# Kernel optimization log

Hardware: AMD Instinct MI355X
Metric: run time of the kernel (lower is better)

The kernel has to match this reference:

```python
import math
import jax, jax.numpy as jnp
import numpy as np


def _unfold(x, kh, kw, dh, dw, ph, pw):
    """F.unfold equivalent: returns (n, c, kh*kw, h, w), channel-major like torch."""
    n, c, h, w = x.shape
    xp = jnp.pad(x, ((0, 0), (0, 0), (ph, ph), (pw, pw)))
    patches = jnp.stack(
        [xp[:, :, i * dh:i * dh + h, j * dw:j * dw + w]
         for i in range(kh) for j in range(kw)],
        axis=2,
    )
    return patches  # (n, c, kh*kw, h, w)


def setup_inputs() -> dict:
    key = jax.random.key(0)
    k1, k2, k3, k4 = jax.random.split(key, 4)
    n, c, h, w = 8, 128, 64, 64
    x = jax.random.normal(k1, (n, c, h, w), dtype=jnp.float32)
    p1_w = 0.1 * jax.random.normal(k2, (1, c, h, 1), dtype=jnp.float32)  # trunc_normal std=0.1
    p7_w = jax.random.normal(k3, (c, c), dtype=jnp.float32) / np.sqrt(c)  # 1x1 conv c->c
    # grouped 1x1 conv: groups=4, out=c*21, weight (c*21, c//4)
    p10_w = jax.random.normal(k4, (c * 21, c // 4), dtype=jnp.float32) / np.sqrt(c // 4)
    return {"x": x, "p1_w": p1_w, "p7_w": p7_w, "p10_w": p10_w}


def reference(x, p1_w, p7_w, p10_w):
    n, c, h, w = x.shape
    g = 4
    t1 = p1_w * x                        # (n,c,h,w)
    t2 = x + t1
    t4 = jax.nn.relu(x)
    t5 = _unfold(x, 3, 7, 1, 1, 1, 3)    # (n,c,21,h,w)
    t7 = jnp.einsum('oc,nchw->nohw', p7_w, t4)        # 1x1 conv
    t8 = _unfold(t7, 1, 5, 1, 3, 0, 6)   # (n,c,5,h,w)
    t9 = x[:, :, None] - t8              # (n,c,5,h,w)
    # grouped 1x1 conv c -> c*21, groups=4
    xg = t2.reshape(n, g, c // g, h, w)
    wg = p10_w.reshape(g, (c * 21) // g, c // g)
    t10 = jnp.einsum('ngihw,goi->ngohw', xg, wg).reshape(n, c * 21, h, w)
    # score: (n,c,hw) x (n,hw,c*21) -> (n,c,c*21)
    t1f = t1.reshape(n, c, h * w)
    t5f = t5.reshape(n, c * 21, h * w)
    t11 = jnp.einsum('nck,nmk->ncm', t1f, t5f) / math.sqrt(h * w)
    t12 = t9.mean(2)                     # (n,c,h,w)
    t13 = jnp.einsum('ncm,nmk->nck', t11, t10.reshape(n, c * 21, h * w))
    t13 = t13.reshape(n, c, h, w) / math.sqrt(c * 21)
    return jnp.maximum(t13, t12)
```

## Files before the change

kernel.cpp:

```cpp
#include <hip/hip_runtime.h>
#include <hip/hip_bf16.h>

typedef unsigned short ushort_t;
typedef unsigned int uint_t;
typedef __attribute__((ext_vector_type(8))) short s16x8;
typedef __attribute__((ext_vector_type(4))) float f32x4;
typedef __attribute__((ext_vector_type(4))) ushort_t u16x4;
typedef __attribute__((ext_vector_type(8))) ushort_t u16x8;

__device__ __forceinline__ ushort_t f2bf(float f) {
    uint_t u = __float_as_uint(f);
    uint_t r = (u + 0x7FFFu + ((u >> 16) & 1u)) >> 16;
    return (ushort_t)r;
}
__device__ __forceinline__ float bf2f(ushort_t u) {
    return __uint_as_float(((uint_t)u) << 16);
}
__device__ __forceinline__ s16x8 relu8(s16x8 v) {
    s16x8 r;
#pragma unroll
    for (int e = 0; e < 8; ++e) { short xv = v[e]; r[e] = (xv < 0) ? (short)0 : xv; }
    return r;
}

__global__ __launch_bounds__(256) void prep_all(const float* __restrict__ x,
                                                const float* __restrict__ p1,
                                                const float* __restrict__ p10,
                                                const float* __restrict__ p7,
                                                ushort_t* __restrict__ t1h,
                                                ushort_t* __restrict__ xpTh,
                                                ushort_t* __restrict__ wfc,
                                                ushort_t* __restrict__ p7h) {
    __shared__ float xs[64][65];
    __shared__ float p1s[64];
    const int b = blockIdx.x;
    const int t = threadIdx.x;
    if (b < 1024) {
        const int y  = b & 63;
        const int c0 = ((b >> 6) & 1) * 64;
        const int n  = b >> 7;
        if (t < 64) p1s[t] = p1[(c0 + t) * 64 + y];
#pragma unroll
        for (int cc = 0; cc < 4; ++cc) {
            int c = cc * 16 + (t >> 4);
            int px = (t & 15) * 4;
            float4 v = *(const float4*)(x + ((size_t)((n * 128 + c0 + c)) * 64 + y) * 64 + px);
            xs[c][px] = v.x; xs[c][px + 1] = v.y; xs[c][px + 2] = v.z; xs[c][px + 3] = v.w;
        }
        __syncthreads();
        {
            int c = t >> 2, px0 = (t & 3) * 16;
            float pv = p1s[c];
            u16x8 o0, o1;
#pragma unroll
            for (int e = 0; e < 8; ++e) {
                o0[e] = f2bf(pv * xs[c][px0 + e]);
                o1[e] = f2bf(pv * xs[c][px0 + 8 + e]);
            }
            ushort_t* dst = t1h + (size_t)(n * 128 + c0 + c) * 4096 + y * 64 + px0;
            *(u16x8*)dst = o0;
            *(u16x8*)(dst + 8) = o1;
        }
        {
            int p = t >> 2, cx0 = (t & 3) * 16;
            u16x8 r0, r1;
#pragma unroll
            for (int e = 0; e < 8; ++e) {
                r0[e] = f2bf(xs[cx0 + e][p]);
                r1[e] = f2bf(xs[cx0 + 8 + e][p]);
            }
            size_t baseP = ((size_t)n * 4752 + (y + 1) * 72 + p + 3) * 128 + c0 + cx0;
            *(u16x8*)(xpTh + baseP) = r0;
            *(u16x8*)(xpTh + baseP + 8) = r1;
        }
    } else {
        int idx = (b - 1024) * 256 + t;
        if (idx < 83968) {
            int chunk = idx & 15;
            int rest  = idx >> 4;
            int n = rest / 656;
            int s = rest - n * 656;
            int yy, xx;
            if (s < 144) { yy = (s < 72) ? 0 : 65; xx = s % 72; }
            else { int s2 = s - 144; yy = (s2 >> 3) + 1; int k = s2 & 7; xx = (k < 3) ? k : k + 64; }
            u16x8 z = {};
            *(u16x8*)(xpTh + ((size_t)n * 4752 + yy * 72 + xx) * 128 + chunk * 8) = z;
        } else if (idx < 83968 + 86016) {
            int i = idx - 83968;
            int c32 = i & 31;
            int j = (i >> 5) & 31;
            int rest = i >> 10;
            int tap = rest % 21, g = rest / 21;
            wfc[i] = f2bf(p10[((32 * g + c32) * 21 + tap) * 32 + j]);
        } else if (idx < 83968 + 86016 + 16384) {
            int i = idx - 83968 - 86016;
            p7h[i] = f2bf(p7[i]);
        }
    }
}

__global__ __launch_bounds__(256) void guf_mfma(const ushort_t* __restrict__ xpTh,
                                                const ushort_t* __restrict__ wfc,
                                                const ushort_t* __restrict__ t1h,
                                                ushort_t* __restrict__ uparth) {
    __shared__ ushort_t Ts[6 * 72 * 32];
    __shared__ ushort_t Gs[32 * 256];
    const int pt = blockIdx.x;
    const int p0 = pt * 256;
    const int g  = blockIdx.y;
    const int n  = blockIdx.z;
    const int tid = threadIdx.x;
    const int lane = tid & 63, wid = tid >> 6;
    const int q = lane >> 4, fr = lane & 15;
    const int y0 = p0 >> 6;

    const ushort_t* src = xpTh + ((size_t)n * 4752 + y0 * 72) * 128 + g * 32;
    for (int flat = tid; flat < 1728; flat += 256) {
        int qq = flat & 3;
        int cc = (flat >> 2) % 72;
        int rr = (flat >> 2) / 72;
        u16x8 v = *(const u16x8*)(src + ((size_t)rr * 72 + cc) * 128 + qq * 8);
        *(u16x8*)&Ts[(rr * 72 + cc) * 32 + ((qq ^ ((cc >> 1) & 3)) * 8)] = v;
    }
    __syncthreads();

    const ushort_t* wbase = wfc + (size_t)g * 21 * 1024 + fr * 32 + q * 8;
    f32x4 acc[2][4] = {};
    for (int tap = 0; tap < 21; ++tap) {
        const int ki = tap / 7, kj = tap - ki * 7;
        s16x8 a[2], b[4];
#pragma unroll
        for (int i = 0; i < 2; ++i)
            a[i] = *(const s16x8*)(wbase + tap * 1024 + i * 16 * 32);
#pragma unroll
        for (int jj = 0; jj < 4; ++jj) {
            int col = wid * 64 + jj * 16 + fr;
            int rr = (col >> 6) + ki;
            int cc = (col & 63) + kj;
            b[jj] = *(const s16x8*)&Ts[(rr * 72 + cc) * 32 + ((q ^ ((cc >> 1) & 3)) * 8)];
        }
#pragma unroll
        for (int i = 0; i < 2; ++i)
#pragma unroll
            for (int jj = 0; jj < 4; ++jj)
                acc[i][jj] = __builtin_amdgcn_mfma_f32_16x16x32_bf16(a[i], b[jj], acc[i][jj], 0, 0, 0);
    }
    const ushort_t* t1base = t1h + (size_t)n * 128 * 4096 + p0;
    const int cb = wid * 32;
    s16x8 bpre[2][2];
#pragma unroll
    for (int kk = 0; kk < 2; ++kk)
#pragma unroll
        for (int l = 0; l < 2; ++l)
            bpre[kk][l] = *(const s16x8*)(t1base + (size_t)(cb + l * 16 + fr) * 4096 + kk * 32 + q * 8);

#pragma unroll
    for (int i = 0; i < 2; ++i) {
#pragma unroll
        for (int jj = 0; jj < 4; ++jj) {
            int p = wid * 64 + jj * 16 + fr;
            int pc = p >> 3, pe = p & 7;
#pragma unroll
            for (int reg = 0; reg < 4; ++reg) {
                int j = i * 16 + q * 4 + reg;
                Gs[j * 256 + ((pc ^ (j & 7)) * 8) + pe] = f2bf(acc[i][jj][reg]);
            }
        }
    }
    __syncthreads();

    f32x4 accu[2][2] = {};
    for (int kk = 0; kk < 8; ++kk) {
        s16x8 a[2], b[2];
#pragma unroll
        for (int i = 0; i < 2; ++i) {
            int j = i * 16 + fr;
            a[i] = *(const s16x8*)&Gs[j * 256 + (((kk * 4 + q) ^ (j & 7)) * 8)];
        }
        if (kk < 2) {
#pragma unroll
            for (int l = 0; l < 2; ++l) b[l] = bpre[kk][l];
        } else {
#pragma unroll
            for (int l = 0; l < 2; ++l)
                b[l] = *(const s16x8*)(t1base + (size_t)(cb + l * 16 + fr) * 4096 + kk * 32 + q * 8);
        }
#pragma unroll
        for (int i = 0; i < 2; ++i)
#pragma unroll
            for (int l = 0; l < 2; ++l)
                accu[i][l] = __builtin_amdgcn_mfma_f32_16x16x32_bf16(a[i], b[l], accu[i][l], 0, 0, 0);
    }
#pragma unroll
    for (int i = 0; i < 2; ++i) {
#pragma unroll
        for (int l = 0; l < 2; ++l) {
            int c = cb + l * 16 + fr;
            u16x4 o;
#pragma unroll
            for (int reg = 0; reg < 4; ++reg) o[reg] = f2bf(accu[i][l][reg]);
            *(u16x4*)&uparth[((size_t)(n * 16 + pt) * 128 + c) * 128 + g * 32 + i * 16 + q * 4] = o;
        }
    }
}

__global__ void ureduce_kernel(const ushort_t* __restrict__ uparth, ushort_t* __restrict__ Uh) {
    int idx = blockIdx.x * 256 + threadIdx.x;
    int n = idx >> 14, rc = idx & 16383;
    float s = 0.0f;
#pragma unroll
    for (int k = 0; k < 16; ++k) s += bf2f(uparth[(size_t)((n * 16 + k) << 14) + rc]);
    Uh[idx] = f2bf(s * 0.015625f);
}

__global__ __launch_bounds__(256) void outf_mfma(const ushort_t* __restrict__ p7h,
                                                 const ushort_t* __restrict__ xpTh,
                                                 const ushort_t* __restrict__ Uh,
                                                 const float* __restrict__ p1,
                                                 float* __restrict__ out) {
    __shared__ ushort_t Bs[8192];
    __shared__ ushort_t Cs[9984];
    __shared__ ushort_t T12s[8192];
    __shared__ float p1s[128];
    const int y = blockIdx.x;
    const int n = blockIdx.y;
    const int tid = threadIdx.x;
    const int lane = tid & 63, w = tid >> 6;
    const int q = lane >> 4, fr = lane & 15;

    if (tid < 128) p1s[tid] = p1[tid * 64 + y];
    int adS[4], chS[4];
#pragma unroll
    for (int it = 0; it < 4; ++it) {
        int slot = it * 256 + tid;
        int row = slot >> 4, ch = slot & 15;
        chS[it] = ch;
        adS[it] = (row * 16 + (ch ^ (row & 15))) * 8;
        u16x8 v = *(const u16x8*)(xpTh + ((size_t)n * 4752 + (y + 1) * 72 + 3 + row) * 128 + ch * 8);
        *(u16x8*)&Bs[adS[it]] = v;
    }
    __syncthreads();

    f32x4 acc[2][4] = {};
    for (int ks = 0; ks < 4; ++ks) {
        s16x8 a[2], b[4];
#pragma unroll
        for (int i = 0; i < 2; ++i)
            a[i] = *(const s16x8*)(p7h + (w * 32 + i * 16 + fr) * 128 + ks * 32 + q * 8);
#pragma unroll
        for (int jj = 0; jj < 4; ++jj) {
            int rb = jj * 16 + fr;
            b[jj] = relu8(*(const s16x8*)&Bs[(rb * 16 + ((ks * 4 + q) ^ (rb & 15))) * 8]);
        }
#pragma unroll
        for (int i = 0; i < 2; ++i)
#pragma unroll
            for (int jj = 0; jj < 4; ++jj)
                acc[i][jj] = __builtin_amdgcn_mfma_f32_16x16x32_bf16(a[i], b[jj], acc[i][jj], 0, 0, 0);
    }
    s16x8 upre[2][4];
#pragma unroll
    for (int i = 0; i < 2; ++i)
#pragma unroll
        for (int ks = 0; ks < 4; ++ks)
            upre[i][ks] = *(const s16x8*)(Uh + ((size_t)(n * 128 + w * 32 + i * 16 + fr)) * 128 + ks * 32 + q * 8);

    for (int i2 = tid; i2 < 4992; i2 += 256) ((uint_t*)Cs)[i2] = 0u;
    __syncthreads();
#pragma unroll
    for (int i = 0; i < 2; ++i)
#pragma unroll
        for (int jj = 0; jj < 4; ++jj) {
            int col = jj * 16 + fr;
#pragma unroll
            for (int reg = 0; reg < 4; ++reg) {
                int row = w * 32 + i * 16 + q * 4 + reg;
                Cs[row * 78 + 6 + col] = f2bf(acc[i][jj][reg]);
            }
        }
    __syncthreads();
    for (int rep = 0; rep < 32; ++rep) {
        int flat = rep * 256 + tid;
        int c = flat >> 6, xx = flat & 63;
        float s = 0.0f;
#pragma unroll
        for (int jj = 0; jj < 5; ++jj)
            s += bf2f(Cs[c * 78 + xx + 3 * jj]);
        float xv = bf2f(Bs[(xx * 16 + ((c >> 3) ^ (xx & 15))) * 8 + (c & 7)]);
        T12s[flat] = f2bf(xv - 0.2f * s);
    }
    __syncthreads();
#pragma unroll
    for (int it = 0; it < 4; ++it) {
        u16x8 v = *(u16x8*)&Bs[adS[it]];
        u16x8 o;
#pragma unroll
        for (int e = 0; e < 8; ++e)
            o[e] = f2bf(bf2f(v[e]) * (1.0f + p1s[chS[it] * 8 + e]));
        *(u16x8*)&Bs[adS[it]] = o;
    }
    __syncthreads();
    f32x4 acc2[2][4] = {};
    for (int ks = 0; ks < 4; ++ks) {
        s16x8 b[4];
#pragma unroll
        for (int jj = 0; jj < 4; ++jj) {
            int rb = jj * 16 + fr;
            b[jj] = *(const s16x8*)&Bs[(rb * 16 + ((ks * 4 + q) ^ (rb & 15))) * 8];
        }
#pragma unroll
        for (int i = 0; i < 2; ++i)
#pragma unroll
            for (int jj = 0; jj < 4; ++jj)
                acc2[i][jj] = __builtin_amdgcn_mfma_f32_16x16x32_bf16(upre[i][ks], b[jj], acc2[i][jj], 0, 0, 0);
    }
    const float scale = 0.0192879257f;
#pragma unroll
    for (int i = 0; i < 2; ++i)
#pragma unroll
        for (int jj = 0; jj < 4; ++jj) {
            int col = jj * 16 + fr;
#pragma unroll
            for (int reg = 0; reg < 4; ++reg) {
                int row = w * 32 + i * 16 + q * 4 + reg;
                size_t oi = ((size_t)(n * 128 + row)) * 4096 + y * 64 + col;
                out[oi] = fmaxf(bf2f(T12s[row * 64 + col]), acc2[i][jj][reg] * scale);
            }
        }
}

extern "C" void kernel_launch(void* const* d_in, const int* in_sizes, int n_in,
                              void* d_out, int out_size, void* d_ws, size_t ws_size,
                              hipStream_t stream) {
    const float* x   = (const float*)d_in[0];
    const float* p1  = (const float*)d_in[1];
    const float* p7  = (const float*)d_in[2];
    const float* p10 = (const float*)d_in[3];
    float* out = (float*)d_out;

    ushort_t* t1h    = (ushort_t*)d_ws;
    ushort_t* xpTh   = t1h + 4194304;
    ushort_t* p7h    = xpTh + 4866048;
    ushort_t* wfc    = p7h + 16384;
    ushort_t* Uh     = wfc + 86016;
    ushort_t* uparth = Uh + 131072;

    prep_all<<<1752, 256, 0, stream>>>(x, p1, p10, p7, t1h, xpTh, wfc, p7h);
    guf_mfma<<<dim3(16, 4, 8), 256, 0, stream>>>(xpTh, wfc, t1h, uparth);
    ureduce_kernel<<<512, 256, 0, stream>>>(uparth, Uh);
    outf_mfma<<<dim3(64, 8), 256, 0, stream>>>(p7h, xpTh, Uh, p1, out);
}
```

Before: 44.91 us.

## Fuse guf, reduce and output kernels into one persistent kernel with flags

Result: slower. 134.3 us (+199.0%).

```diff
diff --git a/kernel.cpp b/kernel.cpp
--- a/kernel.cpp
+++ b/kernel.cpp
@@ -30,7 +30,8 @@
                                                 ushort_t* __restrict__ t1h,
                                                 ushort_t* __restrict__ xpTh,
                                                 ushort_t* __restrict__ wfc,
-                                                ushort_t* __restrict__ p7h) {
+                                                ushort_t* __restrict__ p7h,
+                                                uint_t* __restrict__ flags) {
     __shared__ float xs[64][65];
     __shared__ float p1s[64];
     const int b = blockIdx.x;
@@ -74,6 +75,7 @@
             *(u16x8*)(xpTh + baseP + 8) = r1;
         }
     } else {
+        if (b == 1024 && t < 16) flags[t] = 0u;
         int idx = (b - 1024) * 256 + t;
         if (idx < 83968) {
             int chunk = idx & 15;
@@ -99,234 +101,264 @@
     }
 }
 
-__global__ __launch_bounds__(256) void guf_mfma(const ushort_t* __restrict__ xpTh,
-                                                const ushort_t* __restrict__ wfc,
-                                                const ushort_t* __restrict__ t1h,
-                                                ushort_t* __restrict__ uparth) {
-    __shared__ ushort_t Ts[6 * 72 * 32];
-    __shared__ ushort_t Gs[32 * 256];
-    const int pt = blockIdx.x;
-    const int p0 = pt * 256;
-    const int g  = blockIdx.y;
-    const int n  = blockIdx.z;
+__global__ __launch_bounds__(256, 2) void mega_mfma(const ushort_t* __restrict__ xpTh,
+                                                    const ushort_t* __restrict__ wfc,
+                                                    const ushort_t* __restrict__ t1h,
+                                                    const ushort_t* __restrict__ p7h,
+                                                    const float* __restrict__ p1,
+                                                    ushort_t* __restrict__ uparth,
+                                                    ushort_t* __restrict__ Uh,
+                                                    uint_t* __restrict__ flags,
+                                                    float* __restrict__ out) {
+    __shared__ __align__(16) char smem[53248];
+    __shared__ uint_t sflag;
+    uint_t* cnt  = flags;
+    uint_t* done = flags + 8;
+    const int b = blockIdx.x;
     const int tid = threadIdx.x;
     const int lane = tid & 63, wid = tid >> 6;
     const int q = lane >> 4, fr = lane & 15;
-    const int y0 = p0 >> 6;
-
-    const ushort_t* src = xpTh + ((size_t)n * 4752 + y0 * 72) * 128 + g * 32;
-    for (int flat = tid; flat < 1728; flat += 256) {
-        int qq = flat & 3;
-        int cc = (flat >> 2) % 72;
-        int rr = (flat >> 2) / 72;
-        u16x8 v = *(const u16x8*)(src + ((size_t)rr * 72 + cc) * 128 + qq * 8);
-        *(u16x8*)&Ts[(rr * 72 + cc) * 32 + ((qq ^ ((cc >> 1) & 3)) * 8)] = v;
+
+    {
+        ushort_t* Ts = (ushort_t*)smem;
+        ushort_t* Gs = (ushort_t*)(smem + 27648);
+        const int n_g = b & 7;
+        const int g   = (b >> 3) & 3;
+        const int pt  = b >> 5;
+        const int p0  = pt * 256;
+        const int y0  = p0 >> 6;
+
+        const ushort_t* src = xpTh + ((size_t)n_g * 4752 + y0 * 72) * 128 + g * 32;
+        for (int flat = tid; flat < 1728; flat += 256) {
+            int qq = flat & 3;
+            int cc = (flat >> 2) % 72;
+            int rr = (flat >> 2) / 72;
+            u16x8 v = *(const u16x8*)(src + ((size_t)rr * 72 + cc) * 128 + qq * 8);
+            *(u16x8*)&Ts[(rr * 72 + cc) * 32 + ((qq ^ ((cc >> 1) & 3)) * 8)] = v;
+        }
+        __syncthreads();
+
+        const ushort_t* wbase = wfc + (size_t)g * 21 * 1024 + fr * 32 + q * 8;
+        f32x4 acc[2][4] = {};
+        for (int tap = 0; tap < 21; ++tap) {
+            const int ki = tap / 7, kj = tap - ki * 7;
+            s16x8 a[2], bb[4];
+#pragma unroll
+            for (int i = 0; i < 2; ++i)
+                a[i] = *(const s16x8*)(wbase + tap * 1024 + i * 16 * 32);
+#pragma unroll
+            for (int jj = 0; jj < 4; ++jj) {
+                int col = wid * 64 + jj * 16 + fr;
+                int rr = (col >> 6) + ki;
+                int cc = (col & 63) + kj;
+                bb[jj] = *(const s16x8*)&Ts[(rr * 72 + cc) * 32 + ((q ^ ((cc >> 1) & 3)) * 8)];
+            }
+#pragma unroll
+            for (int i = 0; i < 2; ++i)
+#pragma unroll
+                for (int jj = 0; jj < 4; ++jj)
+                    acc[i][jj] = __builtin_amdgcn_mfma_f32_16x16x32_bf16(a[i], bb[jj], acc[i][jj], 0, 0, 0);
+        }
+        const ushort_t* t1base = t1h + (size_t)n_g * 128 * 4096 + p0;
+        const int cb = wid * 32;
+        s16x8 bpre[2][2];
+#pragma unroll
+        for (int kk = 0; kk < 2; ++kk)
+#pragma unroll
+            for (int l = 0; l < 2; ++l)
+                bpre[kk][l] = *(const s16x8*)(t1base + (size_t)(cb + l * 16 + fr) * 4096 + kk * 32 + q * 8);
+
+#pragma unroll
+        for (int i = 0; i < 2; ++i) {
+#pragma unroll
+            for (int jj = 0; jj < 4; ++jj) {
+                int p = wid * 64 + jj * 16 + fr;
+                int pc = p >> 3, pe = p & 7;
+#pragma unroll
+                for (int reg = 0; reg < 4; ++reg) {
+                    int j = i * 16 + q * 4 + reg;
+                    Gs[j * 256 + ((pc ^ (j & 7)) * 8) + pe] = f2bf(acc[i][jj][reg]);
+                }
+            }
+        }
+        __syncthreads();
+
+        f32x4 accu[2][2] = {};
+        for (int kk = 0; kk < 8; ++kk) {
+            s16x8 a[2], bb[2];
+#pragma unroll
+            for (int i = 0; i < 2; ++i) {
+                int j = i * 16 + fr;
+                a[i] = *(const s16x8*)&Gs[j * 256 + (((kk * 4 + q) ^ (j & 7)) * 8)];
+            }
+            if (kk < 2) {
+#pragma unroll
+                for (int l = 0; l < 2; ++l) bb[l] = bpre[kk][l];
+            } else {
+#pragma unroll
+                for (int l = 0; l < 2; ++l)
+                    bb[l] = *(const s16x8*)(t1base + (size_t)(cb + l * 16 + fr) * 4096 + kk * 32 + q * 8);
+            }
+#pragma unroll
+            for (int i = 0; i < 2; ++i)
+#pragma unroll
+                for (int l = 0; l < 2; ++l)
+                    accu[i][l] = __builtin_amdgcn_mfma_f32_16x16x32_bf16(a[i], bb[l], accu[i][l], 0, 0, 0);
+        }
+#pragma unroll
+        for (int i = 0; i < 2; ++i) {
+#pragma unroll
+            for (int l = 0; l < 2; ++l) {
+                int c = cb + l * 16 + fr;
+                u16x4 o;
+#pragma unroll
+                for (int reg = 0; reg < 4; ++reg) o[reg] = f2bf(accu[i][l][reg]);
+                *(u16x4*)&uparth[((size_t)(n_g * 16 + pt) * 128 + c) * 128 + g * 32 + i * 16 + q * 4] = o;
+            }
+        }
+        __syncthreads();
+        if (tid == 0) {
+            __threadfence();
+            uint_t old = __hip_atomic_fetch_add(&cnt[n_g], 1u, __ATOMIC_ACQ_REL, __HIP_MEMORY_SCOPE_AGENT);
+            sflag = (old == 63u) ? 1u : 0u;
+        }
+        __syncthreads();
+        if (sflag) {
+            for (int i = tid; i < 4096; i += 256) {
+                int rc4 = i * 4;
+                float s0 = 0, s1 = 0, s2 = 0, s3 = 0;
+#pragma unroll
+                for (int k = 0; k < 16; ++k) {
+                    u16x4 v = *(const u16x4*)&uparth[(size_t)((n_g * 16 + k) << 14) + rc4];
+                    s0 += bf2f(v[0]); s1 += bf2f(v[1]); s2 += bf2f(v[2]); s3 += bf2f(v[3]);
+                }
+                u16x4 o;
+                o[0] = f2bf(s0 * 0.015625f); o[1] = f2bf(s1 * 0.015625f);
+                o[2] = f2bf(s2 * 0.015625f); o[3] = f2bf(s3 * 0.015625f);
+                *(u16x4*)&Uh[n_g * 16384 + rc4] = o;
+            }
+            __syncthreads();
+            if (tid == 0) {
+                __threadfence();
+                __hip_atomic_store(&done[n_g], 1u, __ATOMIC_RELEASE, __HIP_MEMORY_SCOPE_AGENT);
+            }
+        }
+    }
+
+    const int n_o = b >> 6;
+    const int y   = b & 63;
+    if (tid == 0) {
+        while (__hip_atomic_load(&done[n_o], __ATOMIC_ACQUIRE, __HIP_MEMORY_SCOPE_AGENT) == 0u)
+            __builtin_amdgcn_s_sleep(8);
     }
     __syncthreads();
-
-    const ushort_t* wbase = wfc + (size_t)g * 21 * 1024 + fr * 32 + q * 8;
-    f32x4 acc[2][4] = {};
-    for (int tap = 0; tap < 21; ++tap) {
-        const int ki = tap / 7, kj = tap - ki * 7;
-        s16x8 a[2], b[4];
+    {
+        ushort_t* Bs   = (ushort_t*)smem;
+        ushort_t* Cs   = (ushort_t*)(smem + 16384);
+        ushort_t* T12s = (ushort_t*)(smem + 36352);
+        float*    p1s  = (float*)(smem + 52736);
+        const int w = wid;
+
+        if (tid < 128) p1s[tid] = p1[tid * 64 + y];
+        int adS[4], chS[4];
+#pragma unroll
+        for (int it = 0; it < 4; ++it) {
+            int slot = it * 256 + tid;
+            int row = slot >> 4, ch = slot & 15;
+            chS[it] = ch;
+            adS[it] = (row * 16 + (ch ^ (row & 15))) * 8;
+            u16x8 v = *(const u16x8*)(xpTh + ((size_t)n_o * 4752 + (y + 1) * 72 + 3 + row) * 128 + ch * 8);
+            *(u16x8*)&Bs[adS[it]] = v;
+        }
+        __syncthreads();
+
+        f32x4 acc[2][4] = {};
+        for (int ks = 0; ks < 4; ++ks) {
+            s16x8 a[2], bb[4];
+#pragma unroll
+            for (int i = 0; i < 2; ++i)
+                a[i] = *(const s16x8*)(p7h + (w * 32 + i * 16 + fr) * 128 + ks * 32 + q * 8);
+#pragma unroll
+            for (int jj = 0; jj < 4; ++jj) {
+                int rb = jj * 16 + fr;
+                bb[jj] = relu8(*(const s16x8*)&Bs[(rb * 16 + ((ks * 4 + q) ^ (rb & 15))) * 8]);
+            }
+#pragma unroll
+            for (int i = 0; i < 2; ++i)
+#pragma unroll
+                for (int jj = 0; jj < 4; ++jj)
+                    acc[i][jj] = __builtin_amdgcn_mfma_f32_16x16x32_bf16(a[i], bb[jj], acc[i][jj], 0, 0, 0);
+        }
+        s16x8 upre[2][4];
 #pragma unroll
         for (int i = 0; i < 2; ++i)
-            a[i] = *(const s16x8*)(wbase + tap * 1024 + i * 16 * 32);
-#pragma unroll
-        for (int jj = 0; jj < 4; ++jj) {
-            int col = wid * 64 + jj * 16 + fr;
-            int rr = (col >> 6) + ki;
-            int cc = (col & 63) + kj;
-            b[jj] = *(const s16x8*)&Ts[(rr * 72 + cc) * 32 + ((q ^ ((cc >> 1) & 3)) * 8)];
-        }
+#pragma unroll
+            for (int ks = 0; ks < 4; ++ks)
+                upre[i][ks] = *(const s16x8*)(Uh + ((size_t)(n_o * 128 + w * 32 + i * 16 + fr)) * 128 + ks * 32 + q * 8);
+
+        for (int i2 = tid; i2 < 4992; i2 += 256) ((uint_t*)Cs)[i2] = 0u;
+        __syncthreads();
 #pragma unroll
         for (int i = 0; i < 2; ++i)
 #pragma unroll
-            for (int jj = 0; jj < 4; ++jj)
-                acc[i][jj] = __builtin_amdgcn_mfma_f32_16x16x32_bf16(a[i], b[jj], acc[i][jj], 0, 0, 0);
+            for (int jj = 0; jj < 4; ++jj) {
+                int col = jj * 16 + fr;
+#pragma unroll
+                for (int reg = 0; reg < 4; ++reg) {
+                    int row = w * 32 + i * 16 + q * 4 + reg;
+                    Cs[row * 78 + 6 + col] = f2bf(acc[i][jj][reg]);
+                }
+            }
+        __syncthreads();
+        for (int rep = 0; rep < 32; ++rep) {
+            int flat = rep * 256 + tid;
+            int c = flat >> 6, xx = flat & 63;
+            float s = 0.0f;
+#pragma unroll
+            for (int jj = 0; jj < 5; ++jj)
+                s += bf2f(Cs[c * 78 + xx + 3 * jj]);
+            float xv = bf2f(Bs[(xx * 16 + ((c >> 3) ^ (xx & 15))) * 8 + (c & 7)]);
+            T12s[flat] = f2bf(xv - 0.2f * s);
+        }
+        __syncthreads();
+#pragma unroll
+        for (int it = 0; it < 4; ++it) {
+            u16x8 v = *(u16x8*)&Bs[adS[it]];
+            u16x8 o;
+#pragma unroll
+            for (int e = 0; e < 8; ++e)
+                o[e] = f2bf(bf2f(v[e]) * (1.0f + p1s[chS[it] * 8 + e]));
+            *(u16x8*)&Bs[adS[it]] = o;
+        }
+        __syncthreads();
+        f32x4 acc2[2][4] = {};
+        for (int ks = 0; ks < 4; ++ks) {
+            s16x8 bb[4];
+#pragma unroll
+            for (int jj = 0; jj < 4; ++jj) {
+                int rb = jj * 16 + fr;
+                bb[jj] = *(const s16x8*)&Bs[(rb * 16 + ((ks * 4 + q) ^ (rb & 15))) * 8];
+            }
+#pragma unroll
+            for (int i = 0; i < 2; ++i)
+#pragma unroll
+                for (int jj = 0; jj < 4; ++jj)
+                    acc2[i][jj] = __builtin_amdgcn_mfma_f32_16x16x32_bf16(upre[i][ks], bb[jj], acc2[i][jj], 0, 0, 0);
+        }
+        const float scale = 0.0192879257f;
+#pragma unroll
+        for (int i = 0; i < 2; ++i)
+#pragma unroll
+            for (int jj = 0; jj < 4; ++jj) {
+                int col = jj * 16 + fr;
+#pragma unroll
+                for (int reg = 0; reg < 4; ++reg) {
+                    int row = w * 32 + i * 16 + q * 4 + reg;
+                    size_t oi = ((size_t)(n_o * 128 + row)) * 4096 + y * 64 + col;
+                    out[oi] = fmaxf(bf2f(T12s[row * 64 + col]), acc2[i][jj][reg] * scale);
+                }
+            }
     }
-    const ushort_t* t1base = t1h + (size_t)n * 128 * 4096 + p0;
-    const int cb = wid * 32;
-    s16x8 bpre[2][2];
-#pragma unroll
-    for (int kk = 0; kk < 2; ++kk)
-#pragma unroll
-        for (int l = 0; l < 2; ++l)
-            bpre[kk][l] = *(const s16x8*)(t1base + (size_t)(cb + l * 16 + fr) * 4096 + kk * 32 + q * 8);
-
-#pragma unroll
-    for (int i = 0; i < 2; ++i) {
-#pragma unroll
-        for (int jj = 0; jj < 4; ++jj) {
-            int p = wid * 64 + jj * 16 + fr;
-            int pc = p >> 3, pe = p & 7;
-#pragma unroll
-            for (int reg = 0; reg < 4; ++reg) {
-                int j = i * 16 + q * 4 + reg;
-                Gs[j * 256 + ((pc ^ (j & 7)) * 8) + pe] = f2bf(acc[i][jj][reg]);
-            }
-        }
-    }
-    __syncthreads();
-
-    f32x4 accu[2][2] = {};
-    for (int kk = 0; kk < 8; ++kk) {
-        s16x8 a[2], b[2];
-#pragma unroll
-        for (int i = 0; i < 2; ++i) {
-            int j = i * 16 + fr;
-            a[i] = *(const s16x8*)&Gs[j * 256 + (((kk * 4 + q) ^ (j & 7)) * 8)];
-        }
-        if (kk < 2) {
-#pragma unroll
-            for (int l = 0; l < 2; ++l) b[l] = bpre[kk][l];
-        } else {
-#pragma unroll
-            for (int l = 0; l < 2; ++l)
-                b[l] = *(const s16x8*)(t1base + (size_t)(cb + l * 16 + fr) * 4096 + kk * 32 + q * 8);
-        }
-#pragma unroll
-        for (int i = 0; i < 2; ++i)
-#pragma unroll
-            for (int l = 0; l < 2; ++l)
-                accu[i][l] = __builtin_amdgcn_mfma_f32_16x16x32_bf16(a[i], b[l], accu[i][l], 0, 0, 0);
-    }
-#pragma unroll
-    for (int i = 0; i < 2; ++i) {
-#pragma unroll
-        for (int l = 0; l < 2; ++l) {
-            int c = cb + l * 16 + fr;
-            u16x4 o;
-#pragma unroll
-            for (int reg = 0; reg < 4; ++reg) o[reg] = f2bf(accu[i][l][reg]);
-            *(u16x4*)&uparth[((size_t)(n * 16 + pt) * 128 + c) * 128 + g * 32 + i * 16 + q * 4] = o;
-        }
-    }
-}
-
-__global__ void ureduce_kernel(const ushort_t* __restrict__ uparth, ushort_t* __restrict__ Uh) {
-    int idx = blockIdx.x * 256 + threadIdx.x;
-    int n = idx >> 14, rc = idx & 16383;
-    float s = 0.0f;
-#pragma unroll
-    for (int k = 0; k < 16; ++k) s += bf2f(uparth[(size_t)((n * 16 + k) << 14) + rc]);
-    Uh[idx] = f2bf(s * 0.015625f);
-}
-
-__global__ __launch_bounds__(256) void outf_mfma(const ushort_t* __restrict__ p7h,
-                                                 const ushort_t* __restrict__ xpTh,
-                                                 const ushort_t* __restrict__ Uh,
-                                                 const float* __restrict__ p1,
-                                                 float* __restrict__ out) {
-    __shared__ ushort_t Bs[8192];
-    __shared__ ushort_t Cs[9984];
-    __shared__ ushort_t T12s[8192];
-    __shared__ float p1s[128];
-    const int y = blockIdx.x;
-    const int n = blockIdx.y;
-    const int tid = threadIdx.x;
-    const int lane = tid & 63, w = tid >> 6;
-    const int q = lane >> 4, fr = lane & 15;
-
-    if (tid < 128) p1s[tid] = p1[tid * 64 + y];
-    int adS[4], chS[4];
-#pragma unroll
-    for (int it = 0; it < 4; ++it) {
-        int slot = it * 256 + tid;
-        int row = slot >> 4, ch = slot & 15;
-        chS[it] = ch;
-        adS[it] = (row * 16 + (ch ^ (row & 15))) * 8;
-        u16x8 v = *(const u16x8*)(xpTh + ((size_t)n * 4752 + (y + 1) * 72 + 3 + row) * 128 + ch * 8);
-        *(u16x8*)&Bs[adS[it]] = v;
-    }
-    __syncthreads();
-
-    f32x4 acc[2][4] = {};
-    for (int ks = 0; ks < 4; ++ks) {
-        s16x8 a[2], b[4];
-#pragma unroll
-        for (int i = 0; i < 2; ++i)
-            a[i] = *(const s16x8*)(p7h + (w * 32 + i * 16 + fr) * 128 + ks * 32 + q * 8);
-#pragma unroll
-        for (int jj = 0; jj < 4; ++jj) {
-            int rb = jj * 16 + fr;
-            b[jj] = relu8(*(const s16x8*)&Bs[(rb * 16 + ((ks * 4 + q) ^ (rb & 15))) * 8]);
-        }
-#pragma unroll
-        for (int i = 0; i < 2; ++i)
-#pragma unroll
-            for (int jj = 0; jj < 4; ++jj)
-                acc[i][jj] = __builtin_amdgcn_mfma_f32_16x16x32_bf16(a[i], b[jj], acc[i][jj], 0, 0, 0);
-    }
-    s16x8 upre[2][4];
-#pragma unroll
-    for (int i = 0; i < 2; ++i)
-#pragma unroll
-        for (int ks = 0; ks < 4; ++ks)
-            upre[i][ks] = *(const s16x8*)(Uh + ((size_t)(n * 128 + w * 32 + i * 16 + fr)) * 128 + ks * 32 + q * 8);
-
-    for (int i2 = tid; i2 < 4992; i2 += 256) ((uint_t*)Cs)[i2] = 0u;
-    __syncthreads();
-#pragma unroll
-    for (int i = 0; i < 2; ++i)
-#pragma unroll
-        for (int jj = 0; jj < 4; ++jj) {
-            int col = jj * 16 + fr;
-#pragma unroll
-            for (int reg = 0; reg < 4; ++reg) {
-                int row = w * 32 + i * 16 + q * 4 + reg;
-                Cs[row * 78 + 6 + col] = f2bf(acc[i][jj][reg]);
-            }
-        }
-    __syncthreads();
-    for (int rep = 0; rep < 32; ++rep) {
-        int flat = rep * 256 + tid;
-        int c = flat >> 6, xx = flat & 63;
-        float s = 0.0f;
-#pragma unroll
-        for (int jj = 0; jj < 5; ++jj)
-            s += bf2f(Cs[c * 78 + xx + 3 * jj]);
-        float xv = bf2f(Bs[(xx * 16 + ((c >> 3) ^ (xx & 15))) * 8 + (c & 7)]);
-        T12s[flat] = f2bf(xv - 0.2f * s);
-    }
-    __syncthreads();
-#pragma unroll
-    for (int it = 0; it < 4; ++it) {
-        u16x8 v = *(u16x8*)&Bs[adS[it]];
-        u16x8 o;
-#pragma unroll
-        for (int e = 0; e < 8; ++e)
-            o[e] = f2bf(bf2f(v[e]) * (1.0f + p1s[chS[it] * 8 + e]));
-        *(u16x8*)&Bs[adS[it]] = o;
-    }
-    __syncthreads();
-    f32x4 acc2[2][4] = {};
-    for (int ks = 0; ks < 4; ++ks) {
-        s16x8 b[4];
-#pragma unroll
-        for (int jj = 0; jj < 4; ++jj) {
-            int rb = jj * 16 + fr;
-            b[jj] = *(const s16x8*)&Bs[(rb * 16 + ((ks * 4 + q) ^ (rb & 15))) * 8];
-        }
-#pragma unroll
-        for (int i = 0; i < 2; ++i)
-#pragma unroll
-            for (int jj = 0; jj < 4; ++jj)
-                acc2[i][jj] = __builtin_amdgcn_mfma_f32_16x16x32_bf16(upre[i][ks], b[jj], acc2[i][jj], 0, 0, 0);
-    }
-    const float scale = 0.0192879257f;
-#pragma unroll
-    for (int i = 0; i < 2; ++i)
-#pragma unroll
-        for (int jj = 0; jj < 4; ++jj) {
-            int col = jj * 16 + fr;
-#pragma unroll
-            for (int reg = 0; reg < 4; ++reg) {
-                int row = w * 32 + i * 16 + q * 4 + reg;
-                size_t oi = ((size_t)(n * 128 + row)) * 4096 + y * 64 + col;
-                out[oi] = fmaxf(bf2f(T12s[row * 64 + col]), acc2[i][jj][reg] * scale);
-            }
-        }
 }
 
 extern "C" void kernel_launch(void* const* d_in, const int* in_sizes, int n_in,
@@ -344,9 +376,8 @@
     ushort_t* wfc    = p7h + 16384;
     ushort_t* Uh     = wfc + 86016;
     ushort_t* uparth = Uh + 131072;
-
-    prep_all<<<1752, 256, 0, stream>>>(x, p1, p10, p7, t1h, xpTh, wfc, p7h);
-    guf_mfma<<<dim3(16, 4, 8), 256, 0, stream>>>(xpTh, wfc, t1h, uparth);
-    ureduce_kernel<<<512, 256, 0, stream>>>(uparth, Uh);
-    outf_mfma<<<dim3(64, 8), 256, 0, stream>>>(p7h, xpTh, Uh, p1, out);
-}
+    uint_t*   flags  = (uint_t*)(uparth + 2097152);
+
+    prep_all<<<1752, 256, 0, stream>>>(x, p1, p10, p7, t1h, xpTh, wfc, p7h, flags);
+    mega_mfma<<<512, 256, 0, stream>>>(xpTh, wfc, t1h, p7h, p1, uparth, Uh, flags, out);
+}
```
